# Performance work log

Hardware: AMD Instinct MI355X
Metric: run time of the kernel (lower is better)

The kernel has to match this reference:

```python
import jax, jax.numpy as jnp
import numpy as np

E, T, D_IN, D_HID, D_OUT = 8, 2048, 1024, 4096, 1024
INTER = 2 * D_HID  # gated (SwiGLU) -> weight1 produces [gate, val]


def setup_inputs() -> dict:
    key = jax.random.key(0)
    k_x, k_w1, k_w2 = jax.random.split(key, 3)
    # kaiming_uniform-ish scale for weights
    x = jax.random.normal(k_x, (E, T, D_IN), dtype=jnp.float32)
    w1 = jax.random.normal(k_w1, (E, D_IN, INTER), dtype=jnp.float32) * (1.0 / np.sqrt(D_IN))
    w2 = jax.random.normal(k_w2, (E, D_HID, D_OUT), dtype=jnp.float32) * (1.0 / np.sqrt(D_HID))
    return {"x": x, "weight1": w1, "weight2": w2}


def reference(x, weight1, weight2):
    # h: [E, T, 2*D_HID] grouped GEMM over experts
    h = jnp.einsum("etd,edi->eti", x, weight1)
    gate, val = jnp.split(h, 2, axis=-1)
    h = jax.nn.silu(gate) * val  # SwiGLU; dropout is identity in eval / p=0
    out = jnp.einsum("eth,eho->eto", h, weight2)  # [E, T, D_OUT]
    return out
```

## Files before the change

kernel.cpp:

```cpp
#include <hip/hip_runtime.h>


#define E_    8
#define T_    2048
#define DIN   1024
#define DHID  4096
#define DOUT  1024
#define INTER 8192

typedef _Float16 f16;
typedef _Float16 f16x8 __attribute__((ext_vector_type(8)));
typedef float    f32x4 __attribute__((ext_vector_type(4)));

typedef const __attribute__((address_space(1))) void gvoid_t;
typedef __attribute__((address_space(3))) void lvoid_t;

__device__ __forceinline__ void gload_lds16(const void* g, void* l) {
  __builtin_amdgcn_global_load_lds((gvoid_t*)g, (lvoid_t*)l, 16, 0, 0);
}

__global__ __launch_bounds__(256) void conv_f32_f16(
    const float* __restrict__ src, f16* __restrict__ dst, int n8) {
  int i = blockIdx.x * 256 + threadIdx.x;
  int stride = gridDim.x * 256;
  for (; i < n8; i += stride) {
    const float4* s = (const float4*)(src + (size_t)i * 8);
    float4 a0 = s[0], a1 = s[1];
    f16x8 v;
    v[0] = (f16)a0.x; v[1] = (f16)a0.y; v[2] = (f16)a0.z; v[3] = (f16)a0.w;
    v[4] = (f16)a1.x; v[5] = (f16)a1.y; v[6] = (f16)a1.z; v[7] = (f16)a1.w;
    *(f16x8*)(dst + (size_t)i * 8) = v;
  }
}

__global__ __launch_bounds__(256) void xpose_f32_f16(
    const float* __restrict__ src, f16* __restrict__ dst,
    int R, int C, int tR, int tC) {
  __shared__ f16 tile[32][33];
  int bid = blockIdx.x;
  int perE = tR * tC;
  int e = bid / perE;
  int rem = bid - e * perE;
  int rt = rem / tC;
  int ct = rem - rt * tC;
  int r0 = rt * 32, c0 = ct * 32;
  int t = threadIdx.x;
  int lr = t >> 5, lc = t & 31;
  const float* s = src + (size_t)e * R * C;
  f16* d = dst + (size_t)e * C * R;
#pragma unroll
  for (int i = 0; i < 4; ++i) {
    int r = lr + 8 * i;
    tile[r][lc] = (f16)s[(size_t)(r0 + r) * C + (c0 + lc)];
  }
  __syncthreads();
#pragma unroll
  for (int i = 0; i < 4; ++i) {
    int r = lr + 8 * i;
    d[(size_t)(c0 + r) * R + (r0 + lc)] = tile[lc][r];
  }
}

__global__ __launch_bounds__(512, 2) void gemm1_swiglu_xh(
    const f16* __restrict__ xh,
    const f16* __restrict__ w1t,
    f16* __restrict__ hact) {
  __shared__ f16 As[128][32];
  __shared__ f16 Bg[128][32];
  __shared__ f16 Bv[128][32];

  int bid = blockIdx.x;
  int e   = bid >> 9;
  int rem = bid & 511;
  int mt  = rem >> 5;
  int nt  = rem & 31;
  int m0 = mt * 128, n0 = nt * 128;

  const f16* xe = xh  + ((size_t)e * T_ + m0) * DIN;
  const f16* wg = w1t + ((size_t)e * INTER + n0) * DIN;
  const f16* wv = w1t + ((size_t)e * INTER + DHID + n0) * DIN;

  int tid  = threadIdx.x;
  int lane = tid & 63;
  int wid  = tid >> 6;

  int srow = wid * 16 + (lane >> 2);
  int scol = (lane & 3) * 8;
  f16* lA = &As[wid * 16][0];
  f16* lG = &Bg[wid * 16][0];
  f16* lV = &Bv[wid * 16][0];

  int wm = wid >> 2;
  int wn = wid & 3;
  int lr = lane & 15;
  int lk = (lane >> 4) * 8;

  f32x4 accG[4][2], accV[4][2];
#pragma unroll
  for (int m = 0; m < 4; ++m)
#pragma unroll
    for (int n = 0; n < 2; ++n) {
      accG[m][n] = f32x4{0.f, 0.f, 0.f, 0.f};
      accV[m][n] = f32x4{0.f, 0.f, 0.f, 0.f};
    }

  for (int k = 0; k < DIN; k += 32) {
    __syncthreads();
    gload_lds16(xe + (size_t)srow * DIN + k + scol, lA);
    gload_lds16(wg + (size_t)srow * DIN + k + scol, lG);
    gload_lds16(wv + (size_t)srow * DIN + k + scol, lV);
    __syncthreads();

    f16x8 af[4], bg[2], bv[2];
#pragma unroll
    for (int m = 0; m < 4; ++m)
      af[m] = *(const f16x8*)&As[wm * 64 + m * 16 + lr][lk];
#pragma unroll
    for (int n = 0; n < 2; ++n) {
      bg[n] = *(const f16x8*)&Bg[wn * 32 + n * 16 + lr][lk];
      bv[n] = *(const f16x8*)&Bv[wn * 32 + n * 16 + lr][lk];
    }
#pragma unroll
    for (int m = 0; m < 4; ++m)
#pragma unroll
      for (int n = 0; n < 2; ++n) {
        accG[m][n] = __builtin_amdgcn_mfma_f32_16x16x32_f16(af[m], bg[n], accG[m][n], 0, 0, 0);
        accV[m][n] = __builtin_amdgcn_mfma_f32_16x16x32_f16(af[m], bv[n], accV[m][n], 0, 0, 0);
      }
  }

  f16* he = hact + (size_t)e * T_ * DHID;
  int rbase = m0 + wm * 64 + (lane >> 4) * 4;
  int cbase = n0 + wn * 32 + lr;
#pragma unroll
  for (int m = 0; m < 4; ++m)
#pragma unroll
    for (int n = 0; n < 2; ++n)
#pragma unroll
      for (int j = 0; j < 4; ++j) {
        int row = rbase + m * 16 + j;
        int col = cbase + n * 16;
        float g = accG[m][n][j];
        float v = accV[m][n][j];
        float s = g / (1.0f + __expf(-g));
        he[(size_t)row * DHID + col] = (f16)(s * v);
      }
}

__global__ __launch_bounds__(512, 2) void gemm1_swiglu_rs(
    const float* __restrict__ x,
    const f16* __restrict__ w1t,
    f16* __restrict__ hact) {
  __shared__ f16 As[128][36];
  __shared__ f16 Bg[128][32];
  __shared__ f16 Bv[128][32];

  int bid = blockIdx.x;
  int e   = bid >> 9;
  int rem = bid & 511;
  int mt  = rem >> 5;
  int nt  = rem & 31;
  int m0 = mt * 128, n0 = nt * 128;

  const float* xe = x   + ((size_t)e * T_ + m0) * DIN;
  const f16*   wg = w1t + ((size_t)e * INTER + n0) * DIN;
  const f16*   wv = w1t + ((size_t)e * INTER + DHID + n0) * DIN;

  int tid  = threadIdx.x;
  int lane = tid & 63;
  int wid  = tid >> 6;

  int arow = tid >> 2;
  int acol = (tid & 3) * 8;
  int brow = wid * 16 + (lane >> 2);
  int bcol = (lane & 3) * 8;
  f16* lG = &Bg[wid * 16][0];
  f16* lV = &Bv[wid * 16][0];

  int wm = wid >> 2;
  int wn = wid & 3;
  int lr = lane & 15;
  int lk = (lane >> 4) * 8;

  f32x4 accG[4][2], accV[4][2];
#pragma unroll
  for (int m = 0; m < 4; ++m)
#pragma unroll
    for (int n = 0; n < 2; ++n) {
      accG[m][n] = f32x4{0.f, 0.f, 0.f, 0.f};
      accV[m][n] = f32x4{0.f, 0.f, 0.f, 0.f};
    }

  for (int k = 0; k < DIN; k += 32) {
    __syncthreads();
    gload_lds16(wg + (size_t)brow * DIN + k + bcol, lG);
    gload_lds16(wv + (size_t)brow * DIN + k + bcol, lV);
    {
      const float* sa = xe + (size_t)arow * DIN + k + acol;
      float4 a0 = ((const float4*)sa)[0];
      float4 a1 = ((const float4*)sa)[1];
      f16x8 v;
      v[0] = (f16)a0.x; v[1] = (f16)a0.y; v[2] = (f16)a0.z; v[3] = (f16)a0.w;
      v[4] = (f16)a1.x; v[5] = (f16)a1.y; v[6] = (f16)a1.z; v[7] = (f16)a1.w;
      *(f16x8*)&As[arow][acol] = v;
    }
    __syncthreads();

    f16x8 af[4], bg[2], bv[2];
#pragma unroll
    for (int m = 0; m < 4; ++m)
      af[m] = *(const f16x8*)&As[wm * 64 + m * 16 + lr][lk];
#pragma unroll
    for (int n = 0; n < 2; ++n) {
      bg[n] = *(const f16x8*)&Bg[wn * 32 + n * 16 + lr][lk];
      bv[n] = *(const f16x8*)&Bv[wn * 32 + n * 16 + lr][lk];
    }
#pragma unroll
    for (int m = 0; m < 4; ++m)
#pragma unroll
      for (int n = 0; n < 2; ++n) {
        accG[m][n] = __builtin_amdgcn_mfma_f32_16x16x32_f16(af[m], bg[n], accG[m][n], 0, 0, 0);
        accV[m][n] = __builtin_amdgcn_mfma_f32_16x16x32_f16(af[m], bv[n], accV[m][n], 0, 0, 0);
      }
  }

  f16* he = hact + (size_t)e * T_ * DHID;
  int rbase = m0 + wm * 64 + (lane >> 4) * 4;
  int cbase = n0 + wn * 32 + lr;
#pragma unroll
  for (int m = 0; m < 4; ++m)
#pragma unroll
    for (int n = 0; n < 2; ++n)
#pragma unroll
      for (int j = 0; j < 4; ++j) {
        int row = rbase + m * 16 + j;
        int col = cbase + n * 16;
        float g = accG[m][n][j];
        float v = accV[m][n][j];
        float s = g / (1.0f + __expf(-g));
        he[(size_t)row * DHID + col] = (f16)(s * v);
      }
}

__global__ __launch_bounds__(512, 2) void gemm2_8ph(
    const f16* __restrict__ hact,
    const f16* __restrict__ w2t,
    float* __restrict__ out) {
  __shared__ __align__(1024) f16 As[2][256][64];
  __shared__ __align__(1024) f16 Bs[2][256][64];

  int bid = blockIdx.x;
  int e   = bid >> 5;
  int rem = bid & 31;
  int mt  = rem >> 2;
  int nt  = rem & 3;
  int m0 = mt * 256, n0 = nt * 256;

  const f16* ha = hact + ((size_t)e * T_ + m0) * DHID;
  const f16* wb = w2t  + ((size_t)e * DOUT + n0) * DHID;

  int tid  = threadIdx.x;
  int lane = tid & 63;
  int wid  = tid >> 6;
  int wm   = wid >> 2;
  int wn   = wid & 3;
  int lr   = lane & 15;
  int l16  = lane >> 4;

  int srow = lane >> 3;
  int scol = ((lane & 7) ^ srow) * 8;

  auto stA = [&](int buf, int kt, int i) {
    int ci = wid + 8 * i;
    gload_lds16(ha + (size_t)(ci * 8 + srow) * DHID + kt * 64 + scol,
                (char*)&As[buf][0][0] + ci * 1024);
  };
  auto stB = [&](int buf, int kt, int i) {
    int ci = wid + 8 * i;
    gload_lds16(wb + (size_t)(ci * 8 + srow) * DHID + kt * 64 + scol,
                (char*)&Bs[buf][0][0] + ci * 1024);
  };

  f32x4 acc[8][4];
#pragma unroll
  for (int m = 0; m < 8; ++m)
#pragma unroll
    for (int n = 0; n < 4; ++n) acc[m][n] = f32x4{0.f, 0.f, 0.f, 0.f};

  f16x8 af[4][2], bf0[2][2], bf1[2][2];

#define READ_A2(b, MH)                                                       \
  _Pragma("unroll") for (int m = 0; m < 4; ++m)                              \
  _Pragma("unroll") for (int kk = 0; kk < 2; ++kk) {                         \
    int row_ = wm * 128 + (MH) * 64 + m * 16 + lr;                           \
    af[m][kk] = *(const f16x8*)((const char*)&As[b][0][0] + row_ * 128 +     \
                                (((kk * 4 + l16) ^ (lr & 7)) << 4));         \
  }
#define READ_B2(b, NH, DST)                                                  \
  _Pragma("unroll") for (int n = 0; n < 2; ++n)                              \
  _Pragma("unroll") for (int kk = 0; kk < 2; ++kk) {                         \
    int row_ = wn * 64 + (NH) * 32 + n * 16 + lr;                            \
    DST[n][kk] = *(const f16x8*)((const char*)&Bs[b][0][0] + row_ * 128 +    \
                                 (((kk * 4 + l16) ^ (lr & 7)) << 4));        \
  }
#define MFMA16Q(MH, NH, BB)                                                  \
  __builtin_amdgcn_s_setprio(1);                                            \
  _Pragma("unroll") for (int m = 0; m < 4; ++m)                              \
  _Pragma("unroll") for (int n = 0; n < 2; ++n)                              \
  _Pragma("unroll") for (int kk = 0; kk < 2; ++kk)                          \
    acc[(MH) * 4 + m][(NH) * 2 + n] = __builtin_amdgcn_mfma_f32_16x16x32_f16(\
        af[m][kk], BB[n][kk], acc[(MH) * 4 + m][(NH) * 2 + n], 0, 0, 0);     \
  __builtin_amdgcn_s_setprio(0);
#define BAR() __builtin_amdgcn_s_barrier()
#define LGKM0() asm volatile("s_waitcnt lgkmcnt(0)" ::: "memory")
#define VM6() asm volatile("s_waitcnt vmcnt(6)" ::: "memory")

  stA(0, 0, 0); stA(0, 0, 1); stA(0, 0, 2); stA(0, 0, 3);
  stB(0, 0, 0); stB(0, 0, 1); stB(0, 0, 2); stB(0, 0, 3);
  stB(1, 1, 0); stB(1, 1, 1); stB(1, 1, 2); stB(1, 1, 3);
  stA(1, 1, 0); stA(1, 1, 1);
  VM6();
  BAR();

  for (int it = 0; it < 32; ++it) {
    int tb = 2 * it + 1;
    int pa = (2 * it + 2) & 63;
    int pb = (2 * it + 3) & 63;

    READ_A2(0, 0); READ_B2(0, 0, bf0);
    stA(1, tb, 2); stA(1, tb, 3);
    BAR(); LGKM0();
    MFMA16Q(0, 0, bf0);
    BAR();

    READ_B2(0, 1, bf1);
    BAR(); LGKM0();
    MFMA16Q(0, 1, bf1);
    BAR();

    READ_A2(0, 1);
    stB(0, pa, 0); stB(0, pa, 1);
    BAR(); LGKM0();
    MFMA16Q(1, 0, bf0);
    BAR();

    stB(0, pa, 2); stB(0, pa, 3);
    stA(0, pa, 0); stA(0, pa, 1);
    BAR();
    MFMA16Q(1, 1, bf1);
    VM6();
    BAR();

    READ_A2(1, 0); READ_B2(1, 0, bf0);
    stA(0, pa, 2); stA(0, pa, 3);
    BAR(); LGKM0();
    MFMA16Q(0, 0, bf0);
    BAR();

    READ_B2(1, 1, bf1);
    BAR(); LGKM0();
    MFMA16Q(0, 1, bf1);
    BAR();

    READ_A2(1, 1);
    stB(1, pb, 0); stB(1, pb, 1);
    BAR(); LGKM0();
    MFMA16Q(1, 0, bf0);
    BAR();

    stB(1, pb, 2); stB(1, pb, 3);
    stA(1, pb, 0); stA(1, pb, 1);
    BAR();
    MFMA16Q(1, 1, bf1);
    VM6();
    BAR();
  }

#undef READ_A2
#undef READ_B2
#undef MFMA16Q
#undef BAR
#undef LGKM0
#undef VM6

  float* oe = out + (size_t)e * T_ * DOUT;
  int rbase = m0 + wm * 128 + l16 * 4;
  int cbase = n0 + wn * 64 + lr;
#pragma unroll
  for (int m = 0; m < 8; ++m)
#pragma unroll
    for (int n = 0; n < 4; ++n)
#pragma unroll
      for (int j = 0; j < 4; ++j) {
        int row = rbase + m * 16 + j;
        int col = cbase + n * 16;
        oe[(size_t)row * DOUT + col] = acc[m][n][j];
      }
}

extern "C" void kernel_launch(void* const* d_in, const int* in_sizes, int n_in,
                              void* d_out, int out_size, void* d_ws, size_t ws_size,
                              hipStream_t stream) {
  const float* x  = (const float*)d_in[0];
  const float* w1 = (const float*)d_in[1];
  const float* w2 = (const float*)d_in[2];
  float* out = (float*)d_out;

  const size_t HACT_B = (size_t)E_ * T_ * DHID * 2;
  const size_t WT_B   = (size_t)E_ * INTER * DIN * 2;
  const size_t XH_B   = (size_t)E_ * T_ * DIN * 2;

  f16* hact = (f16*)d_ws;
  f16* wt   = (f16*)((char*)d_ws + HACT_B);

  xpose_f32_f16<<<E_ * (DIN / 32) * (INTER / 32), 256, 0, stream>>>(
      w1, wt, DIN, INTER, DIN / 32, INTER / 32);

  if (ws_size >= HACT_B + WT_B + XH_B) {
    f16* xxh = (f16*)((char*)d_ws + HACT_B + WT_B);
    conv_f32_f16<<<2048, 256, 0, stream>>>(x, xxh, E_ * T_ * DIN / 8);
    gemm1_swiglu_xh<<<E_ * 16 * 32, 512, 0, stream>>>(xxh, wt, hact);
  } else {
    gemm1_swiglu_rs<<<E_ * 16 * 32, 512, 0, stream>>>(x, wt, hact);
  }

  xpose_f32_f16<<<E_ * (DHID / 32) * (DOUT / 32), 256, 0, stream>>>(
      w2, wt, DHID, DOUT, DHID / 32, DOUT / 32);
  gemm2_8ph<<<E_ * 8 * 4, 512, 0, stream>>>(hact, wt, out);
}
```

Baseline: 600.4 us.

## Use 32x32 MFMA in gate GEMM and vectorize 64x64 weight transpose

The first grouped GEMM now uses 32x32x16 MFMA tiles instead of 16x16x32, which cuts the LDS fragment reads per FLOP and changes the accumulator layout and epilogue indexing. The weight transpose kernel is rewritten to use 64x64 tiles with float4 loads and 16-byte f16x8 stores, replacing scalar accesses. Both are meant to cut memory and LDS instruction overhead. The new transpose's LDS read pattern (column reads with a padded row stride) may cause bank conflicts.

```diff
diff --git a/kernel.cpp b/kernel.cpp
--- a/kernel.cpp
+++ b/kernel.cpp
@@ -11,6 +11,7 @@
 typedef _Float16 f16;
 typedef _Float16 f16x8 __attribute__((ext_vector_type(8)));
 typedef float    f32x4 __attribute__((ext_vector_type(4)));
+typedef float    f32x16 __attribute__((ext_vector_type(16)));
 
 typedef const __attribute__((address_space(1))) void gvoid_t;
 typedef __attribute__((address_space(3))) void lvoid_t;
@@ -33,32 +34,38 @@
   }
 }
 
-__global__ __launch_bounds__(256) void xpose_f32_f16(
+__global__ __launch_bounds__(256) void xpose64_f32_f16(
     const float* __restrict__ src, f16* __restrict__ dst,
-    int R, int C, int tR, int tC) {
-  __shared__ f16 tile[32][33];
+    int R, int C, int tC) {
+  __shared__ f16 tile[64][72];
   int bid = blockIdx.x;
-  int perE = tR * tC;
+  int perE = (R >> 6) * tC;
   int e = bid / perE;
   int rem = bid - e * perE;
   int rt = rem / tC;
   int ct = rem - rt * tC;
-  int r0 = rt * 32, c0 = ct * 32;
+  int r0 = rt << 6, c0 = ct << 6;
   int t = threadIdx.x;
-  int lr = t >> 5, lc = t & 31;
-  const float* s = src + (size_t)e * R * C;
-  f16* d = dst + (size_t)e * C * R;
+  int lr  = t >> 2;
+  int lc4 = (t & 3) * 16;
+  const float* s = src + (size_t)e * R * C + (size_t)(r0 + lr) * C + c0 + lc4;
 #pragma unroll
   for (int i = 0; i < 4; ++i) {
-    int r = lr + 8 * i;
-    tile[r][lc] = (f16)s[(size_t)(r0 + r) * C + (c0 + lc)];
+    float4 v = *(const float4*)(s + i * 4);
+    tile[lr][lc4 + i * 4 + 0] = (f16)v.x;
+    tile[lr][lc4 + i * 4 + 1] = (f16)v.y;
+    tile[lr][lc4 + i * 4 + 2] = (f16)v.z;
+    tile[lr][lc4 + i * 4 + 3] = (f16)v.w;
   }
   __syncthreads();
-#pragma unroll
-  for (int i = 0; i < 4; ++i) {
-    int r = lr + 8 * i;
-    d[(size_t)(c0 + r) * R + (r0 + lc)] = tile[lc][r];
-  }
+  f16* d = dst + (size_t)e * C * R + (size_t)(c0 + lr) * R + r0 + lc4;
+  f16x8 o0, o1;
+#pragma unroll
+  for (int j = 0; j < 8; ++j) o0[j] = tile[lc4 + j][lr];
+#pragma unroll
+  for (int j = 0; j < 8; ++j) o1[j] = tile[lc4 + 8 + j][lr];
+  *(f16x8*)(d)     = o0;
+  *(f16x8*)(d + 8) = o1;
 }
 
 __global__ __launch_bounds__(512, 2) void gemm1_swiglu_xh(
@@ -90,19 +97,17 @@
   f16* lG = &Bg[wid * 16][0];
   f16* lV = &Bv[wid * 16][0];
 
-  int wm = wid >> 2;
-  int wn = wid & 3;
-  int lr = lane & 15;
-  int lk = (lane >> 4) * 8;
-
-  f32x4 accG[4][2], accV[4][2];
-#pragma unroll
-  for (int m = 0; m < 4; ++m)
-#pragma unroll
-    for (int n = 0; n < 2; ++n) {
-      accG[m][n] = f32x4{0.f, 0.f, 0.f, 0.f};
-      accV[m][n] = f32x4{0.f, 0.f, 0.f, 0.f};
-    }
+  int wm  = wid >> 2;
+  int wn  = wid & 3;
+  int l31 = lane & 31;
+  int lk2 = (lane >> 5) * 8;
+
+  f32x16 accG[2], accV[2];
+#pragma unroll
+  for (int m = 0; m < 2; ++m) {
+#pragma unroll
+    for (int j = 0; j < 16; ++j) { accG[m][j] = 0.f; accV[m][j] = 0.f; }
+  }
 
   for (int k = 0; k < DIN; k += 32) {
     __syncthreads();
@@ -111,40 +116,41 @@
     gload_lds16(wv + (size_t)srow * DIN + k + scol, lV);
     __syncthreads();
 
-    f16x8 af[4], bg[2], bv[2];
-#pragma unroll
-    for (int m = 0; m < 4; ++m)
-      af[m] = *(const f16x8*)&As[wm * 64 + m * 16 + lr][lk];
-#pragma unroll
-    for (int n = 0; n < 2; ++n) {
-      bg[n] = *(const f16x8*)&Bg[wn * 32 + n * 16 + lr][lk];
-      bv[n] = *(const f16x8*)&Bv[wn * 32 + n * 16 + lr][lk];
+    f16x8 af[2][2], bg2[2], bv2[2];
+#pragma unroll
+    for (int mf = 0; mf < 2; ++mf)
+#pragma unroll
+      for (int kh = 0; kh < 2; ++kh)
+        af[mf][kh] = *(const f16x8*)&As[wm * 64 + mf * 32 + l31][kh * 16 + lk2];
+#pragma unroll
+    for (int kh = 0; kh < 2; ++kh) {
+      bg2[kh] = *(const f16x8*)&Bg[wn * 32 + l31][kh * 16 + lk2];
+      bv2[kh] = *(const f16x8*)&Bv[wn * 32 + l31][kh * 16 + lk2];
     }
 #pragma unroll
-    for (int m = 0; m < 4; ++m)
-#pragma unroll
-      for (int n = 0; n < 2; ++n) {
-        accG[m][n] = __builtin_amdgcn_mfma_f32_16x16x32_f16(af[m], bg[n], accG[m][n], 0, 0, 0);
-        accV[m][n] = __builtin_amdgcn_mfma_f32_16x16x32_f16(af[m], bv[n], accV[m][n], 0, 0, 0);
+    for (int mf = 0; mf < 2; ++mf)
+#pragma unroll
+      for (int kh = 0; kh < 2; ++kh) {
+        accG[mf] = __builtin_amdgcn_mfma_f32_32x32x16_f16(af[mf][kh], bg2[kh], accG[mf], 0, 0, 0);
+        accV[mf] = __builtin_amdgcn_mfma_f32_32x32x16_f16(af[mf][kh], bv2[kh], accV[mf], 0, 0, 0);
       }
   }
 
   f16* he = hact + (size_t)e * T_ * DHID;
-  int rbase = m0 + wm * 64 + (lane >> 4) * 4;
-  int cbase = n0 + wn * 32 + lr;
-#pragma unroll
-  for (int m = 0; m < 4; ++m)
-#pragma unroll
-    for (int n = 0; n < 2; ++n)
-#pragma unroll
-      for (int j = 0; j < 4; ++j) {
-        int row = rbase + m * 16 + j;
-        int col = cbase + n * 16;
-        float g = accG[m][n][j];
-        float v = accV[m][n][j];
-        float s = g / (1.0f + __expf(-g));
-        he[(size_t)row * DHID + col] = (f16)(s * v);
-      }
+  int lhi = lane >> 5;
+  int col = n0 + wn * 32 + l31;
+#pragma unroll
+  for (int mf = 0; mf < 2; ++mf) {
+    int rb = m0 + wm * 64 + mf * 32 + 4 * lhi;
+#pragma unroll
+    for (int r = 0; r < 16; ++r) {
+      int row = rb + (r & 3) + 8 * (r >> 2);
+      float g = accG[mf][r];
+      float v = accV[mf][r];
+      float s = g / (1.0f + __expf(-g));
+      he[(size_t)row * DHID + col] = (f16)(s * v);
+    }
+  }
 }
 
 __global__ __launch_bounds__(512, 2) void gemm1_swiglu_rs(
@@ -413,8 +419,8 @@
   f16* hact = (f16*)d_ws;
   f16* wt   = (f16*)((char*)d_ws + HACT_B);
 
-  xpose_f32_f16<<<E_ * (DIN / 32) * (INTER / 32), 256, 0, stream>>>(
-      w1, wt, DIN, INTER, DIN / 32, INTER / 32);
+  xpose64_f32_f16<<<E_ * (DIN / 64) * (INTER / 64), 256, 0, stream>>>(
+      w1, wt, DIN, INTER, INTER / 64);
 
   if (ws_size >= HACT_B + WT_B + XH_B) {
     f16* xxh = (f16*)((char*)d_ws + HACT_B + WT_B);
@@ -424,7 +430,7 @@
     gemm1_swiglu_rs<<<E_ * 16 * 32, 512, 0, stream>>>(x, wt, hact);
   }
 
-  xpose_f32_f16<<<E_ * (DHID / 32) * (DOUT / 32), 256, 0, stream>>>(
-      w2, wt, DHID, DOUT, DHID / 32, DOUT / 32);
+  xpose64_f32_f16<<<E_ * (DHID / 64) * (DOUT / 64), 256, 0, stream>>>(
+      w2, wt, DHID, DOUT, DOUT / 64);
   gemm2_8ph<<<E_ * 8 * 4, 512, 0, stream>>>(hact, wt, out);
 }
```

New measurement: 652.7 us. 1.09x slower.
